# Performance work log

Hardware: AMD Instinct MI355X
Metric: run time of the kernel (lower is better)

The kernel has to match this reference:

```python
import jax, jax.numpy as jnp
import numpy as np

B, N, D, H = 2, 2048, 1024, 16
HD = D // H
SCALE = HD ** -0.5


def setup_inputs() -> dict:
    key = jax.random.key(0)
    ks = jax.random.split(key, 9)
    s = D ** -0.5
    return {
        "x": jax.random.normal(ks[0], (B, N, D), dtype=jnp.float32),
        "Wq": jax.random.normal(ks[1], (D, D), dtype=jnp.float32) * s,
        "bq": jax.random.normal(ks[2], (D,), dtype=jnp.float32) * 0.01,
        "Wk": jax.random.normal(ks[3], (D, D), dtype=jnp.float32) * s,
        "bk": jax.random.normal(ks[4], (D,), dtype=jnp.float32) * 0.01,
        "Wv": jax.random.normal(ks[5], (D, D), dtype=jnp.float32) * s,
        "bv": jax.random.normal(ks[6], (D,), dtype=jnp.float32) * 0.01,
        "Wo": jax.random.normal(ks[7], (D, D), dtype=jnp.float32) * s,
        "bo": jax.random.normal(ks[8], (D,), dtype=jnp.float32) * 0.01,
    }


def reference(x, Wq, bq, Wk, bk, Wv, bv, Wo, bo):
    # Q/K/V projections (torch Linear: x @ W.T + b), split into heads: (B,H,N,HD)
    def proj(W, b):
        return (x @ W.T + b).reshape(B, N, H, HD).transpose(0, 2, 1, 3)

    q = proj(Wq, bq)
    k = proj(Wk, bk)
    v = proj(Wv, bv)
    # Scaled dot-product attention with explicit (B,H,N,N) scores
    scores = jnp.einsum("bhnd,bhmd->bhnm", q, k) * SCALE
    attn = jax.nn.softmax(scores, axis=-1)
    y = jnp.einsum("bhnm,bhmd->bhnd", attn, v)
    y = y.transpose(0, 2, 1, 3).reshape(B, N, D)
    # Output projection
    return y @ Wo.T + bo
```

## Files before the change

### kernel.cpp

```cpp
#include <hip/hip_runtime.h>

#define BB 2
#define NN 2048
#define DD 1024
#define HH 16
#define HD 64
#define SCALE 0.125f

typedef unsigned short u16;
typedef unsigned int u32;
typedef __attribute__((ext_vector_type(2))) unsigned int u32x2;
typedef __attribute__((ext_vector_type(4))) short short4v;
typedef __attribute__((ext_vector_type(8))) short short8;
typedef __attribute__((ext_vector_type(4))) float float4v;
typedef __attribute__((ext_vector_type(16))) float f32x16;

__device__ __forceinline__ float b2f(u16 u) {
    union { float f; u32 i; } x; x.i = ((u32)u) << 16; return x.f;
}
__device__ __forceinline__ u16 f2b(float f) {
    union { float f; u32 i; } x; x.f = f;
    u32 i = x.i;
    return (u16)((i + 0x7fffu + ((i >> 16) & 1u)) >> 16);
}

#if __has_builtin(__builtin_amdgcn_exp2f)
#define EXP2F(x) __builtin_amdgcn_exp2f(x)
#else
#define EXP2F(x) __expf((x) * 0.69314718055994531f)
#endif

#if __has_builtin(__builtin_amdgcn_rcpf)
#define RCPF(x) __builtin_amdgcn_rcpf(x)
#else
#define RCPF(x) (1.0f / (x))
#endif

#if __has_builtin(__builtin_amdgcn_permlane32_swap)
#define PSWAP(a, b, ra, rb)                                                  \
    { u32x2 _r = __builtin_amdgcn_permlane32_swap((a), (b), false, false);   \
      (ra) = _r[0]; (rb) = _r[1]; }
#else
#define PSWAP(a, b, ra, rb)                                                  \
    { u32 _xa = (u32)__shfl_xor((int)(a), 32, 64);                           \
      u32 _xb = (u32)__shfl_xor((int)(b), 32, 64);                           \
      (ra) = hi ? _xb : (a); (rb) = hi ? (b) : _xa; }
#endif

__device__ __forceinline__ u32 cvtpk(float a, float b) {
    u32 r;
    asm("v_cvt_pk_bf16_f32 %0, %1, %2" : "=v"(r) : "v"(a), "v"(b));
    return r;
}

__device__ __forceinline__ void gl_lds16(const u16* g, u16* l) {
    __builtin_amdgcn_global_load_lds(
        (__attribute__((address_space(1))) void*)(void*)g,
        (__attribute__((address_space(3))) void*)l, 16, 0, 0);
}

__global__ __launch_bounds__(256) void cvt_all(
    const float* __restrict__ x,
    const float* __restrict__ Wq, const float* __restrict__ Wk,
    const float* __restrict__ Wv, const float* __restrict__ Wo,
    u16* __restrict__ xb, u16* __restrict__ W4)
{
    int e = (blockIdx.x * 256 + threadIdx.x) * 8;
    const float* s;
    u16* d;
    if (e < 4194304) { s = x + e; d = xb + e; }
    else {
        int e2 = e - 4194304;
        int which = e2 >> 20;
        int off = e2 & 1048575;
        s = ((which == 0) ? Wq : (which == 1) ? Wk : (which == 2) ? Wv : Wo) + off;
        d = W4 + e2;
    }
    float4v a = *(const float4v*)s;
    float4v b = *(const float4v*)(s + 4);
    short8 r;
    r[0] = (short)f2b(a[0]); r[1] = (short)f2b(a[1]);
    r[2] = (short)f2b(a[2]); r[3] = (short)f2b(a[3]);
    r[4] = (short)f2b(b[0]); r[5] = (short)f2b(b[1]);
    r[6] = (short)f2b(b[2]); r[7] = (short)f2b(b[3]);
    *(short8*)d = r;
}

__global__ __launch_bounds__(512) void gemm_qkv(
    const u16* __restrict__ xb,
    const u16* __restrict__ Wqb, const float* __restrict__ bq,
    const u16* __restrict__ Wkb, const float* __restrict__ bk,
    const u16* __restrict__ Wvb, const float* __restrict__ bv,
    u16* __restrict__ Qo, u16* __restrict__ Ko, u16* __restrict__ Vt)
{
    const int tn = blockIdx.x;
    const int tm = blockIdx.y;
    const int mat = tn >> 2;
    const int tnq = tn & 3;

    const u16* __restrict__ W     = (mat == 0) ? Wqb : (mat == 1) ? Wkb : Wvb;
    const float* __restrict__ bias = (mat == 0) ? bq : (mat == 1) ? bk : bv;

    __shared__ u16 As[3][256 * 32];
    __shared__ u16 Bs[3][256 * 32];

    const int tid  = threadIdx.x;
    const int wave = tid >> 6, lane = tid & 63;
    const int wm = wave >> 2, wn = wave & 3;
    const int quad = lane >> 4, l16 = lane & 15;

    const int sr = tid >> 2, sc = tid & 3;
    const u16* ga0 = &xb[(size_t)(tm * 256 + sr) * DD + sc * 8];
    const u16* ga1 = ga0 + (size_t)128 * DD;
    const u16* gb0 = &W [(size_t)(tnq * 256 + sr) * DD + sc * 8];
    const u16* gb1 = gb0 + (size_t)128 * DD;

    float4v acc[8][4] = {};

    gl_lds16(ga0,      &As[0][tid * 8]);
    gl_lds16(ga1,      &As[0][(512 + tid) * 8]);
    gl_lds16(gb0,      &Bs[0][tid * 8]);
    gl_lds16(gb1,      &Bs[0][(512 + tid) * 8]);
    gl_lds16(ga0 + 32, &As[1][tid * 8]);
    gl_lds16(ga1 + 32, &As[1][(512 + tid) * 8]);
    gl_lds16(gb0 + 32, &Bs[1][tid * 8]);
    gl_lds16(gb1 + 32, &Bs[1][(512 + tid) * 8]);

    int cb = 0, b2 = 2;
    for (int it = 0; it < 32; ++it) {
        asm volatile("s_waitcnt vmcnt(4)" ::: "memory");
        __builtin_amdgcn_s_barrier();

        const int k2 = ((it + 2) & 31) << 5;
        gl_lds16(ga0 + k2, &As[b2][tid * 8]);
        gl_lds16(ga1 + k2, &As[b2][(512 + tid) * 8]);
        gl_lds16(gb0 + k2, &Bs[b2][tid * 8]);
        gl_lds16(gb1 + k2, &Bs[b2][(512 + tid) * 8]);

        short8 af[8], bf[4];
        #pragma unroll
        for (int mi = 0; mi < 8; ++mi)
            af[mi] = *(const short8*)&As[cb][(wm * 128 + mi * 16 + l16) * 32 + quad * 8];
        #pragma unroll
        for (int ni = 0; ni < 4; ++ni)
            bf[ni] = *(const short8*)&Bs[cb][(wn * 64 + ni * 16 + l16) * 32 + quad * 8];

        #pragma unroll
        for (int mi = 0; mi < 8; ++mi)
            #pragma unroll
            for (int ni = 0; ni < 4; ++ni)
                acc[mi][ni] = __builtin_amdgcn_mfma_f32_16x16x32_bf16(
                    af[mi], bf[ni], acc[mi][ni], 0, 0, 0);

        cb = (cb == 2) ? 0 : cb + 1;
        b2 = (b2 == 2) ? 0 : b2 + 1;
    }
    asm volatile("s_waitcnt vmcnt(0)" ::: "memory");

    #pragma unroll
    for (int mi = 0; mi < 8; ++mi) {
        #pragma unroll
        for (int ni = 0; ni < 4; ++ni) {
            int cc = tnq * 256 + wn * 64 + ni * 16 + l16;
            int h = cc >> 6, hd = cc & 63;
            float bv_ = bias[cc];
            if (mat == 2) {
                short4v v4;
                #pragma unroll
                for (int rr = 0; rr < 4; ++rr)
                    v4[rr] = (short)f2b(acc[mi][ni][rr] + bv_);
                int R0 = tm * 256 + wm * 128 + mi * 16 + quad * 4;
                int b = R0 >> 11, n = R0 & 2047;
                *(short4v*)&Vt[(((size_t)(b * HH + h)) * HD + hd) * NN + n] = v4;
            } else {
                u16* Out = (mat == 0) ? Qo : Ko;
                #pragma unroll
                for (int rr = 0; rr < 4; ++rr) {
                    int R = tm * 256 + wm * 128 + mi * 16 + quad * 4 + rr;
                    int b = R >> 11, n = R & 2047;
                    Out[(((size_t)(b * HH + h)) * NN + n) * HD + hd] =
                        f2b(acc[mi][ni][rr] + bv_);
                }
            }
        }
    }
}

__global__ __launch_bounds__(256) void gemm_out(
    const u16* __restrict__ A, const u16* __restrict__ W,
    const float* __restrict__ bias, float* __restrict__ Out)
{
    const int tm = blockIdx.y;
    const int tn = blockIdx.x;

    __shared__ u16 As[3][64 * 32];
    __shared__ u16 Bs[3][128 * 32];

    const int tid  = threadIdx.x;
    const int wave = tid >> 6, lane = tid & 63;
    const int quad = lane >> 4, l16 = lane & 15;
    const int wn = wave;

    const int r0 = tid >> 2, c0 = tid & 3;

    const u16* ga  = &A[(size_t)(tm * 64 + r0) * DD + c0 * 8];
    const u16* gb0 = &W[(size_t)(tn * 128 + r0) * DD + c0 * 8];
    const u16* gb1 = &W[(size_t)(tn * 128 + r0 + 64) * DD + c0 * 8];

    float4v acc[4][2] = {};

    gl_lds16(ga,       &As[0][tid * 8]);
    gl_lds16(gb0,      &Bs[0][tid * 8]);
    gl_lds16(gb1,      &Bs[0][(256 + tid) * 8]);
    gl_lds16(ga + 32,  &As[1][tid * 8]);
    gl_lds16(gb0 + 32, &Bs[1][tid * 8]);
    gl_lds16(gb1 + 32, &Bs[1][(256 + tid) * 8]);

    int cb = 0, b2 = 2;
    for (int it = 0; it < 32; ++it) {
        asm volatile("s_waitcnt vmcnt(3)" ::: "memory");
        __builtin_amdgcn_s_barrier();

        const int k2 = ((it + 2) & 31) << 5;
        gl_lds16(ga + k2,  &As[b2][tid * 8]);
        gl_lds16(gb0 + k2, &Bs[b2][tid * 8]);
        gl_lds16(gb1 + k2, &Bs[b2][(256 + tid) * 8]);

        short8 af[4], bf[2];
        #pragma unroll
        for (int mi = 0; mi < 4; ++mi)
            af[mi] = *(const short8*)&As[cb][(mi * 16 + l16) * 32 + quad * 8];
        #pragma unroll
        for (int ni = 0; ni < 2; ++ni)
            bf[ni] = *(const short8*)&Bs[cb][(wn * 32 + ni * 16 + l16) * 32 + quad * 8];

        #pragma unroll
        for (int mi = 0; mi < 4; ++mi)
            #pragma unroll
            for (int ni = 0; ni < 2; ++ni)
                acc[mi][ni] = __builtin_amdgcn_mfma_f32_16x16x32_bf16(
                    af[mi], bf[ni], acc[mi][ni], 0, 0, 0);

        cb = (cb == 2) ? 0 : cb + 1;
        b2 = (b2 == 2) ? 0 : b2 + 1;
    }
    asm volatile("s_waitcnt vmcnt(0)" ::: "memory");

    #pragma unroll
    for (int mi = 0; mi < 4; ++mi) {
        #pragma unroll
        for (int ni = 0; ni < 2; ++ni) {
            int cc = tn * 128 + wn * 32 + ni * 16 + l16;
            float bv_ = bias[cc];
            #pragma unroll
            for (int rr = 0; rr < 4; ++rr) {
                int R = tm * 64 + mi * 16 + quad * 4 + rr;
                Out[(size_t)R * DD + cc] = acc[mi][ni][rr] + bv_;
            }
        }
    }
}

__global__ __launch_bounds__(256) void attn_mfma(
    const u16* __restrict__ Q, const u16* __restrict__ K,
    const u16* __restrict__ Vt, u16* __restrict__ Y)
{
    const int id   = blockIdx.x;
    const int xcd  = id & 7;
    const int slot = id >> 3;
    const int bh   = (xcd << 2) | (slot & 3);
    const int qb   = slot >> 2;

    const int tid  = threadIdx.x;
    const int wave = tid >> 6, lane = tid & 63;
    const int l31  = lane & 31, hi = lane >> 5;

    const u16* __restrict__ Qb = Q + (size_t)bh * NN * HD;
    const u16* __restrict__ Kb = K + (size_t)bh * NN * HD;
    const u16* __restrict__ Vb = Vt + (size_t)bh * HD * NN;

    __shared__ u16 Ks[2][64 * 64];
    __shared__ u16 Vs[2][64 * 64];

    short8 qf[4];
    {
        int qrow = qb * 128 + wave * 32 + l31;
        #pragma unroll
        for (int c = 0; c < 4; ++c) {
            short8 t = *(const short8*)&Qb[(size_t)qrow * HD + c * 16 + hi * 8];
            #pragma unroll
            for (int j = 0; j < 8; ++j)
                qf[c][j] = (short)f2b(b2f((u16)t[j]) * SCALE);
        }
    }

    short8 onesB;
    #pragma unroll
    for (int j = 0; j < 8; ++j) onesB[j] = (short)0x3F80;

    f32x16 oc[2] = {};
    f32x16 la = {};

    const int srow = tid >> 3, sslot = tid & 7;
    const int oA = (sslot + srow) & 7;
    const int oB = (sslot + srow + 32) & 7;

    gl_lds16(&Kb[(size_t)srow * HD + oA * 8],          &Ks[0][tid * 8]);
    gl_lds16(&Kb[(size_t)(srow + 32) * HD + oB * 8],   &Ks[0][(256 + tid) * 8]);
    gl_lds16(&Vb[(size_t)srow * NN + oA * 8],          &Vs[0][tid * 8]);
    gl_lds16(&Vb[(size_t)(srow + 32) * NN + oB * 8],   &Vs[0][(256 + tid) * 8]);

    for (int k0 = 0; k0 < NN; k0 += 64) {
        const int cur = (k0 >> 6) & 1;
        const int kn = (k0 + 64) & (NN - 1);

        __syncthreads();

        gl_lds16(&Kb[(size_t)(kn + srow) * HD + oA * 8],      &Ks[cur ^ 1][tid * 8]);
        gl_lds16(&Kb[(size_t)(kn + srow + 32) * HD + oB * 8], &Ks[cur ^ 1][(256 + tid) * 8]);
        gl_lds16(&Vb[(size_t)srow * NN + kn + oA * 8],        &Vs[cur ^ 1][tid * 8]);
        gl_lds16(&Vb[(size_t)(srow + 32) * NN + kn + oB * 8], &Vs[cur ^ 1][(256 + tid) * 8]);

        f32x16 st[2];
        __builtin_amdgcn_s_setprio(1);
        #pragma unroll
        for (int kt = 0; kt < 2; ++kt) {
            f32x16 z = {};
            const int row = kt * 32 + l31;
            #pragma unroll
            for (int c = 0; c < 4; ++c) {
                short8 kf = *(const short8*)
                    &Ks[cur][row * 64 + ((2 * c + hi - row) & 7) * 8];
                z = __builtin_amdgcn_mfma_f32_32x32x16_bf16(kf, qf[c], z, 0, 0, 0);
            }
            st[kt] = z;
        }
        __builtin_amdgcn_s_setprio(0);

        u32 pk0[8], pk1[8];
        #pragma unroll
        for (int i = 0; i < 8; ++i) {
            float a0 = EXP2F(__builtin_fmaf(st[0][2 * i],     1.44269504f, -11.5415603f));
            float a1 = EXP2F(__builtin_fmaf(st[0][2 * i + 1], 1.44269504f, -11.5415603f));
            pk0[i] = cvtpk(a0, a1);
            float b0 = EXP2F(__builtin_fmaf(st[1][2 * i],     1.44269504f, -11.5415603f));
            float b1 = EXP2F(__builtin_fmaf(st[1][2 * i + 1], 1.44269504f, -11.5415603f));
            pk1[i] = cvtpk(b0, b1);
        }

        short8 pa[4];
        {
            union { u32 w[4]; short8 s; } lo, hi_;
            PSWAP(pk0[0], pk0[2], lo.w[0], lo.w[2]);
            PSWAP(pk0[1], pk0[3], lo.w[1], lo.w[3]);
            PSWAP(pk0[4], pk0[6], hi_.w[0], hi_.w[2]);
            PSWAP(pk0[5], pk0[7], hi_.w[1], hi_.w[3]);
            pa[0] = lo.s; pa[1] = hi_.s;
            PSWAP(pk1[0], pk1[2], lo.w[0], lo.w[2]);
            PSWAP(pk1[1], pk1[3], lo.w[1], lo.w[3]);
            PSWAP(pk1[4], pk1[6], hi_.w[0], hi_.w[2]);
            PSWAP(pk1[5], pk1[7], hi_.w[1], hi_.w[3]);
            pa[2] = lo.s; pa[3] = hi_.s;
        }

        __builtin_amdgcn_s_setprio(1);
        #pragma unroll
        for (int ks = 0; ks < 4; ++ks)
            la = __builtin_amdgcn_mfma_f32_32x32x16_bf16(pa[ks], onesB, la, 0, 0, 0);
        #pragma unroll
        for (int ks = 0; ks < 4; ++ks) {
            #pragma unroll
            for (int ht = 0; ht < 2; ++ht) {
                const int row = ht * 32 + l31;
                short8 vf = *(const short8*)
                    &Vs[cur][row * 64 + ((2 * ks + hi - row) & 7) * 8];
                oc[ht] = __builtin_amdgcn_mfma_f32_32x32x16_bf16(pa[ks], vf, oc[ht], 0, 0, 0);
            }
        }
        __builtin_amdgcn_s_setprio(0);
    }
    asm volatile("s_waitcnt vmcnt(0)" ::: "memory");

    const int b = bh >> 4, h = bh & 15;
    #pragma unroll
    for (int r = 0; r < 16; ++r) {
        const int n = qb * 128 + wave * 32 + (r & 3) + 8 * (r >> 2) + 4 * hi;
        const float iv = RCPF(la[r]);
        #pragma unroll
        for (int ht = 0; ht < 2; ++ht) {
            const int col = h * HD + ht * 32 + l31;
            Y[((size_t)(b * NN + n)) * DD + col] = f2b(oc[ht][r] * iv);
        }
    }
}

extern "C" void kernel_launch(void* const* d_in, const int* in_sizes, int n_in,
                              void* d_out, int out_size, void* d_ws, size_t ws_size,
                              hipStream_t stream) {
    const float* x  = (const float*)d_in[0];
    const float* Wq = (const float*)d_in[1];
    const float* bq = (const float*)d_in[2];
    const float* Wk = (const float*)d_in[3];
    const float* bk = (const float*)d_in[4];
    const float* Wv = (const float*)d_in[5];
    const float* bv = (const float*)d_in[6];
    const float* Wo = (const float*)d_in[7];
    const float* bo = (const float*)d_in[8];
    float* out = (float*)d_out;

    const size_t M1 = 1024 * 1024;
    u16* base = (u16*)d_ws;
    u16* xb  = base;
    u16* W4  = base + 4 * M1;
    u16* Wqb = W4;
    u16* Wkb = W4 + 1 * M1;
    u16* Wvb = W4 + 2 * M1;
    u16* Wob = W4 + 3 * M1;
    u16* Qw  = base + 8 * M1;
    u16* Kw  = base + 12 * M1;
    u16* Vtw = base + 16 * M1;
    u16* Yw  = xb;

    cvt_all<<<dim3(4096), 256, 0, stream>>>(x, Wq, Wk, Wv, Wo, xb, W4);

    gemm_qkv<<<dim3(12, 16), 512, 0, stream>>>(xb, Wqb, bq, Wkb, bk, Wvb, bv,
                                               Qw, Kw, Vtw);

    attn_mfma<<<dim3(512), 256, 0, stream>>>(Qw, Kw, Vtw, Yw);

    gemm_out<<<dim3(8, 64), 256, 0, stream>>>(Yw, Wob, bo, out);
}
```

Before: 211.3 us.

## Deepen GEMM LDS pipeline to four stages and remap QKV block order

```diff
diff --git a/kernel.cpp b/kernel.cpp
--- a/kernel.cpp
+++ b/kernel.cpp
@@ -93,16 +93,18 @@
     const u16* __restrict__ Wvb, const float* __restrict__ bv,
     u16* __restrict__ Qo, u16* __restrict__ Ko, u16* __restrict__ Vt)
 {
-    const int tn = blockIdx.x;
-    const int tm = blockIdx.y;
+    const int lid = blockIdx.y * 12 + blockIdx.x;
+    const int seq = (lid & 7) * 24 + (lid >> 3);
+    const int tm = seq / 12;
+    const int tn = seq % 12;
     const int mat = tn >> 2;
     const int tnq = tn & 3;
 
     const u16* __restrict__ W     = (mat == 0) ? Wqb : (mat == 1) ? Wkb : Wvb;
     const float* __restrict__ bias = (mat == 0) ? bq : (mat == 1) ? bk : bv;
 
-    __shared__ u16 As[3][256 * 32];
-    __shared__ u16 Bs[3][256 * 32];
+    __shared__ u16 As[4][256 * 32];
+    __shared__ u16 Bs[4][256 * 32];
 
     const int tid  = threadIdx.x;
     const int wave = tid >> 6, lane = tid & 63;
@@ -117,26 +119,27 @@
 
     float4v acc[8][4] = {};
 
-    gl_lds16(ga0,      &As[0][tid * 8]);
-    gl_lds16(ga1,      &As[0][(512 + tid) * 8]);
-    gl_lds16(gb0,      &Bs[0][tid * 8]);
-    gl_lds16(gb1,      &Bs[0][(512 + tid) * 8]);
-    gl_lds16(ga0 + 32, &As[1][tid * 8]);
-    gl_lds16(ga1 + 32, &As[1][(512 + tid) * 8]);
-    gl_lds16(gb0 + 32, &Bs[1][tid * 8]);
-    gl_lds16(gb1 + 32, &Bs[1][(512 + tid) * 8]);
-
-    int cb = 0, b2 = 2;
+    #pragma unroll
+    for (int s = 0; s < 3; ++s) {
+        const int ks = s << 5;
+        gl_lds16(ga0 + ks, &As[s][tid * 8]);
+        gl_lds16(ga1 + ks, &As[s][(512 + tid) * 8]);
+        gl_lds16(gb0 + ks, &Bs[s][tid * 8]);
+        gl_lds16(gb1 + ks, &Bs[s][(512 + tid) * 8]);
+    }
+
     for (int it = 0; it < 32; ++it) {
-        asm volatile("s_waitcnt vmcnt(4)" ::: "memory");
+        asm volatile("s_waitcnt vmcnt(8)" ::: "memory");
         __builtin_amdgcn_s_barrier();
 
-        const int k2 = ((it + 2) & 31) << 5;
-        gl_lds16(ga0 + k2, &As[b2][tid * 8]);
-        gl_lds16(ga1 + k2, &As[b2][(512 + tid) * 8]);
-        gl_lds16(gb0 + k2, &Bs[b2][tid * 8]);
-        gl_lds16(gb1 + k2, &Bs[b2][(512 + tid) * 8]);
-
+        const int k3 = ((it + 3) & 31) << 5;
+        const int b3 = (it + 3) & 3;
+        gl_lds16(ga0 + k3, &As[b3][tid * 8]);
+        gl_lds16(ga1 + k3, &As[b3][(512 + tid) * 8]);
+        gl_lds16(gb0 + k3, &Bs[b3][tid * 8]);
+        gl_lds16(gb1 + k3, &Bs[b3][(512 + tid) * 8]);
+
+        const int cb = it & 3;
         short8 af[8], bf[4];
         #pragma unroll
         for (int mi = 0; mi < 8; ++mi)
@@ -151,9 +154,6 @@
             for (int ni = 0; ni < 4; ++ni)
                 acc[mi][ni] = __builtin_amdgcn_mfma_f32_16x16x32_bf16(
                     af[mi], bf[ni], acc[mi][ni], 0, 0, 0);
-
-        cb = (cb == 2) ? 0 : cb + 1;
-        b2 = (b2 == 2) ? 0 : b2 + 1;
     }
     asm volatile("s_waitcnt vmcnt(0)" ::: "memory");
 
@@ -193,8 +193,8 @@
     const int tm = blockIdx.y;
     const int tn = blockIdx.x;
 
-    __shared__ u16 As[3][64 * 32];
-    __shared__ u16 Bs[3][128 * 32];
+    __shared__ u16 As[4][64 * 32];
+    __shared__ u16 Bs[4][128 * 32];
 
     const int tid  = threadIdx.x;
     const int wave = tid >> 6, lane = tid & 63;
@@ -209,23 +209,25 @@
 
     float4v acc[4][2] = {};
 
-    gl_lds16(ga,       &As[0][tid * 8]);
-    gl_lds16(gb0,      &Bs[0][tid * 8]);
-    gl_lds16(gb1,      &Bs[0][(256 + tid) * 8]);
-    gl_lds16(ga + 32,  &As[1][tid * 8]);
-    gl_lds16(gb0 + 32, &Bs[1][tid * 8]);
-    gl_lds16(gb1 + 32, &Bs[1][(256 + tid) * 8]);
-
-    int cb = 0, b2 = 2;
+    #pragma unroll
+    for (int s = 0; s < 3; ++s) {
+        const int ks = s << 5;
+        gl_lds16(ga + ks,  &As[s][tid * 8]);
+        gl_lds16(gb0 + ks, &Bs[s][tid * 8]);
+        gl_lds16(gb1 + ks, &Bs[s][(256 + tid) * 8]);
+    }
+
     for (int it = 0; it < 32; ++it) {
-        asm volatile("s_waitcnt vmcnt(3)" ::: "memory");
+        asm volatile("s_waitcnt vmcnt(6)" ::: "memory");
         __builtin_amdgcn_s_barrier();
 
-        const int k2 = ((it + 2) & 31) << 5;
-        gl_lds16(ga + k2,  &As[b2][tid * 8]);
-        gl_lds16(gb0 + k2, &Bs[b2][tid * 8]);
-        gl_lds16(gb1 + k2, &Bs[b2][(256 + tid) * 8]);
-
+        const int k3 = ((it + 3) & 31) << 5;
+        const int b3 = (it + 3) & 3;
+        gl_lds16(ga + k3,  &As[b3][tid * 8]);
+        gl_lds16(gb0 + k3, &Bs[b3][tid * 8]);
+        gl_lds16(gb1 + k3, &Bs[b3][(256 + tid) * 8]);
+
+        const int cb = it & 3;
         short8 af[4], bf[2];
         #pragma unroll
         for (int mi = 0; mi < 4; ++mi)
@@ -240,9 +242,6 @@
             for (int ni = 0; ni < 2; ++ni)
                 acc[mi][ni] = __builtin_amdgcn_mfma_f32_16x16x32_bf16(
                     af[mi], bf[ni], acc[mi][ni], 0, 0, 0);
-
-        cb = (cb == 2) ? 0 : cb + 1;
-        b2 = (b2 == 2) ? 0 : b2 + 1;
     }
     asm volatile("s_waitcnt vmcnt(0)" ::: "memory");
 
```

New measurement: 206.7 us. 1.02x faster.
